# Optimization experiments

Measured on AMD Instinct MI355X. Metric: run time of the kernel, lower is better.

The kernel has to match this reference:

```python
import jax, jax.numpy as jnp
import numpy as np

EPS = 1e-6
LAMBDA_INIT = 0.8

def rmsnorm(x, g):
    return x * jax.lax.rsqrt(jnp.mean(x * x, axis=-1, keepdims=True) + EPS) * g

def diff_attention(q_in, kv_in, Wq, Wk, Wv, Wo, lq1, lk1, lq2, lk2, causal):
    # q_in: [B,T,D], kv_in: [B,S,D]; Wq/Wk: [D, H*2*hs], Wv: [D, H*hs], Wo: [H*hs, D]
    B, T, _ = q_in.shape
    S = kv_in.shape[1]
    H, hs = lq1.shape
    q = (q_in @ Wq).reshape(B, T, H, 2, hs)
    k = (kv_in @ Wk).reshape(B, S, H, 2, hs)
    v = (kv_in @ Wv).reshape(B, S, H, hs)
    q1, q2 = q[..., 0, :], q[..., 1, :]
    k1, k2 = k[..., 0, :], k[..., 1, :]
    scale = 1.0 / np.sqrt(hs).astype(np.float32)
    a1 = jnp.einsum('bthd,bshd->bhts', q1, k1) * scale  # [B,H,T,S]
    a2 = jnp.einsum('bthd,bshd->bhts', q2, k2) * scale
    if causal:
        mask = jnp.tril(jnp.ones((T, S), dtype=bool))
        neg = jnp.asarray(-1e9, a1.dtype)
        a1 = jnp.where(mask, a1, neg)
        a2 = jnp.where(mask, a2, neg)
    s1 = jax.nn.softmax(a1, axis=-1)
    s2 = jax.nn.softmax(a2, axis=-1)
    lam = jnp.exp(jnp.sum(lq1 * lk1, -1)) - jnp.exp(jnp.sum(lq2 * lk2, -1)) + LAMBDA_INIT  # [H]
    attn = s1 - lam[None, :, None, None] * s2
    o = jnp.einsum('bhts,bshd->bthd', attn, v)  # [B,T,H,hs]
    # per-head RMSNorm (no affine) scaled by (1 - lambda_init), per Diff Transformer
    o = o * jax.lax.rsqrt(jnp.mean(o * o, -1, keepdims=True) + EPS) * (1.0 - LAMBDA_INIT)
    return o.reshape(B, T, H * hs) @ Wo

def swiglu(x, W1, W2, W3):
    return (jax.nn.silu(x @ W1) * (x @ W2)) @ W3

def setup_inputs():
    B, T, D, H, hs = 4, 1024, 1024, 16, 64
    Dff = 4 * D
    ks = jax.random.split(jax.random.key(0), 24)
    w = lambda i, shape, s=0.02: (jax.random.normal(ks[i], shape, jnp.float32) * s)
    return {
        'x': jax.random.normal(ks[0], (B, T, D), jnp.float32),
        'encoder_output': jax.random.normal(ks[1], (B, T, D), jnp.float32),
        'Wq_s': w(2, (D, H * 2 * hs)), 'Wk_s': w(3, (D, H * 2 * hs)),
        'Wv_s': w(4, (D, H * hs)), 'Wo_s': w(5, (H * hs, D)),
        'lq1_s': w(6, (H, hs), 0.1), 'lk1_s': w(7, (H, hs), 0.1),
        'lq2_s': w(8, (H, hs), 0.1), 'lk2_s': w(9, (H, hs), 0.1),
        'Wq_c': w(10, (D, H * 2 * hs)), 'Wk_c': w(11, (D, H * 2 * hs)),
        'Wv_c': w(12, (D, H * hs)), 'Wo_c': w(13, (H * hs, D)),
        'lq1_c': w(14, (H, hs), 0.1), 'lk1_c': w(15, (H, hs), 0.1),
        'lq2_c': w(16, (H, hs), 0.1), 'lk2_c': w(17, (H, hs), 0.1),
        'g_rms': jnp.ones((D,), jnp.float32),
        'W1': w(18, (D, Dff)), 'W2': w(19, (D, Dff)), 'W3': w(20, (Dff, D)),
    }

def reference(x, encoder_output, Wq_s, Wk_s, Wv_s, Wo_s, lq1_s, lk1_s, lq2_s, lk2_s,
              Wq_c, Wk_c, Wv_c, Wo_c, lq1_c, lk1_c, lq2_c, lk2_c,
              g_rms, W1, W2, W3):
    # dropout prob 0.0 -> identity (eval/reference mode)
    h = rmsnorm(x, g_rms)
    h = diff_attention(h, h, Wq_s, Wk_s, Wv_s, Wo_s, lq1_s, lk1_s, lq2_s, lk2_s, causal=True) + h
    h = diff_attention(h, encoder_output, Wq_c, Wk_c, Wv_c, Wo_c, lq1_c, lk1_c, lq2_c, lk2_c, causal=False)
    h = h + h  # faithful to source: out = dropout(out) + out after cross-attention
    h = swiglu(rmsnorm(h, g_rms), W1, W2, W3) + h
    return h
```

## Files before the change

### kernel.cpp

```cpp
#include <hip/hip_runtime.h>

typedef __attribute__((ext_vector_type(8))) short s16x8;
typedef __attribute__((ext_vector_type(4))) float f32x4;
typedef unsigned short u16;

__device__ __forceinline__ float bu2f(u16 u) {
    union { unsigned int i; float f; } x; x.i = ((unsigned int)u) << 16; return x.f;
}
__device__ __forceinline__ u16 f2bu(float f) {
    union { float f; unsigned int i; } x; x.f = f;
    unsigned int r = x.i + 0x7fffu + ((x.i >> 16) & 1u);
    return (u16)(r >> 16);
}

__device__ __forceinline__ void gld_lds16(const void* g, void* l) {
    __builtin_amdgcn_global_load_lds(
        (const __attribute__((address_space(1))) unsigned int*)g,
        (__attribute__((address_space(3))) unsigned int*)l, 16, 0, 0);
}
#define WAIT_VM0()   asm volatile("s_waitcnt vmcnt(0)" ::: "memory")
#define WAIT_LGKM0() asm volatile("s_waitcnt lgkmcnt(0)" ::: "memory")
#define MEMBAR()     asm volatile("" ::: "memory")

__global__ __launch_bounds__(256)
void transpose4_k(const float* s0, const float* s1, const float* s2, const float* s3,
                  u16* d0, u16* d1, u16* d2, u16* d3, int R, int C) {
    const float* src = blockIdx.z == 0 ? s0 : blockIdx.z == 1 ? s1 : blockIdx.z == 2 ? s2 : s3;
    u16* dst = blockIdx.z == 0 ? d0 : blockIdx.z == 1 ? d1 : blockIdx.z == 2 ? d2 : d3;
    __shared__ u16 t[32][33];
    int bx = blockIdx.x * 32, by = blockIdx.y * 32;
    int x = bx + threadIdx.x;
#pragma unroll
    for (int k = 0; k < 4; ++k)
        t[threadIdx.y + k * 8][threadIdx.x] = f2bu(src[(size_t)(by + threadIdx.y + k * 8) * C + x]);
    __syncthreads();
    int x2 = by + threadIdx.x;
#pragma unroll
    for (int k = 0; k < 4; ++k)
        dst[(size_t)(bx + threadIdx.y + k * 8) * R + x2] = t[threadIdx.x][threadIdx.y + k * 8];
}

__global__ __launch_bounds__(256)
void convert_k(const float* __restrict__ a, u16* __restrict__ o, int n4) {
    int i = blockIdx.x * 256 + threadIdx.x;
    if (i >= n4) return;
    float4 v = ((const float4*)a)[i];
    ushort4 u;
    u.x = f2bu(v.x); u.y = f2bu(v.y); u.z = f2bu(v.z); u.w = f2bu(v.w);
    ((ushort4*)o)[i] = u;
}

__global__ __launch_bounds__(256)
void rmsnorm_k(const float* __restrict__ x, const float* __restrict__ g, u16* __restrict__ y) {
    const int row = blockIdx.x, tid = threadIdx.x;
    float4 v = ((const float4*)(x + (size_t)row * 1024))[tid];
    float ss = v.x * v.x + v.y * v.y + v.z * v.z + v.w * v.w;
#pragma unroll
    for (int off = 32; off; off >>= 1) ss += __shfl_xor(ss, off, 64);
    __shared__ float red[4];
    if ((tid & 63) == 0) red[tid >> 6] = ss;
    __syncthreads();
    float tot = red[0] + red[1] + red[2] + red[3];
    float sc = rsqrtf(tot * (1.f / 1024.f) + 1e-6f);
    float4 gv = ((const float4*)g)[tid];
    ushort4 o;
    o.x = f2bu(v.x * sc * gv.x);
    o.y = f2bu(v.y * sc * gv.y);
    o.z = f2bu(v.z * sc * gv.z);
    o.w = f2bu(v.w * sc * gv.w);
    ((ushort4*)(y + (size_t)row * 1024))[tid] = o;
}

__global__ __launch_bounds__(256)
void silumul_k(const u16* __restrict__ a, const u16* __restrict__ b, u16* __restrict__ o, int n4) {
    int i = blockIdx.x * 256 + threadIdx.x;
    if (i >= n4) return;
    ushort4 ua = ((const ushort4*)a)[i], ub = ((const ushort4*)b)[i];
    ushort4 uo;
    {
        float v = bu2f(ua.x); uo.x = f2bu(v / (1.f + __expf(-v)) * bu2f(ub.x));
        v = bu2f(ua.y); uo.y = f2bu(v / (1.f + __expf(-v)) * bu2f(ub.y));
        v = bu2f(ua.z); uo.z = f2bu(v / (1.f + __expf(-v)) * bu2f(ub.z));
        v = bu2f(ua.w); uo.w = f2bu(v / (1.f + __expf(-v)) * bu2f(ub.w));
    }
    ((ushort4*)o)[i] = uo;
}

template <int TM>
__global__ __launch_bounds__(256, 2)
void gemm_bt(const u16* __restrict__ A, const u16* __restrict__ Bt, void* __restrict__ C,
             const void* __restrict__ res, int M, int N, int K, int mode) {
    constexpr int MI = TM / 32;
    __shared__ u16 sA[TM * 32];
    __shared__ u16 sB[128 * 32];
    const int tid = threadIdx.x;
    const int w = tid >> 6, lane = tid & 63, q4 = lane >> 4, l16 = lane & 15;
    const int m0 = blockIdx.y * TM, n0 = blockIdx.x * 128;
    const int wm = (w >> 1) * (TM / 2), wn = (w & 1) * 64;

    const f32x4 fzero = {0.f, 0.f, 0.f, 0.f};
    f32x4 acc[MI][4];
#pragma unroll
    for (int i = 0; i < MI; ++i)
#pragma unroll
        for (int j = 0; j < 4; ++j) acc[i][j] = fzero;

    const int r0 = tid >> 2, c0 = (tid & 3) * 8;

    for (int k0 = 0; k0 < K; k0 += 32) {
        gld_lds16(A + (size_t)(m0 + r0) * K + k0 + c0, &sA[tid * 8]);
        if (TM == 128)
            gld_lds16(A + (size_t)(m0 + 64 + r0) * K + k0 + c0, &sA[(256 + tid) * 8]);
        gld_lds16(Bt + (size_t)(n0 + r0) * K + k0 + c0, &sB[tid * 8]);
        gld_lds16(Bt + (size_t)(n0 + 64 + r0) * K + k0 + c0, &sB[(256 + tid) * 8]);
        WAIT_VM0();
        __syncthreads();
        s16x8 af[MI], bfr[4];
#pragma unroll
        for (int i = 0; i < MI; ++i) af[i] = *(const s16x8*)&sA[(wm + i * 16 + l16) * 32 + q4 * 8];
#pragma unroll
        for (int j = 0; j < 4; ++j) bfr[j] = *(const s16x8*)&sB[(wn + j * 16 + l16) * 32 + q4 * 8];
#pragma unroll
        for (int i = 0; i < MI; ++i)
#pragma unroll
            for (int j = 0; j < 4; ++j)
                acc[i][j] = __builtin_amdgcn_mfma_f32_16x16x32_bf16(af[i], bfr[j], acc[i][j], 0, 0, 0);
        __syncthreads();
    }

    const size_t QBSZ = (size_t)4096 * 2048;
    const size_t FSZ  = (size_t)4096 * 4096;
#pragma unroll
    for (int i = 0; i < MI; ++i)
#pragma unroll
        for (int j = 0; j < 4; ++j)
#pragma unroll
            for (int r = 0; r < 4; ++r) {
                int m = m0 + wm + i * 16 + q4 * 4 + r;
                int n = n0 + wn + j * 16 + l16;
                float v = acc[i][j][r];
                if (mode == 0) {
                    ((u16*)C)[(size_t)m * N + n] = f2bu(v);
                } else if (mode == 1) {
                    ((u16*)C)[(size_t)m * N + n] = f2bu(v + bu2f(((const u16*)res)[(size_t)m * N + n]));
                } else if (mode == 2) {
                    ((float*)C)[(size_t)m * N + n] = 2.f * v;
                } else if (mode == 4) {
                    ((float*)C)[(size_t)m * N + n] = v + ((const float*)res)[(size_t)m * N + n];
                } else if (mode == 5) {
                    if (n < 2048) ((u16*)C)[(size_t)m * 2048 + n] = f2bu(v);
                    else if (n < 4096) ((u16*)C)[QBSZ + (size_t)m * 2048 + (n - 2048)] = f2bu(v);
                    else {
                        int nn = n - 4096, hh = nn >> 6, d = nn & 63, b = m >> 10, s = m & 1023;
                        ((u16*)C)[2 * QBSZ + ((size_t)((b * 16 + hh) * 64 + d)) * 1024 + s] = f2bu(v);
                    }
                } else if (mode == 6) {
                    if (n < 2048) ((u16*)C)[(size_t)m * 2048 + n] = f2bu(v);
                    else {
                        int nn = n - 2048, hh = nn >> 6, d = nn & 63, b = m >> 10, s = m & 1023;
                        ((u16*)C)[QBSZ + ((size_t)((b * 16 + hh) * 64 + d)) * 1024 + s] = f2bu(v);
                    }
                } else {
                    if (n < 4096) ((u16*)C)[(size_t)m * 4096 + n] = f2bu(v);
                    else ((u16*)C)[FSZ + (size_t)m * 4096 + (n - 4096)] = f2bu(v);
                }
            }
}

template <bool CAUSAL>
__global__ __launch_bounds__(256, 2)
void diff_flash(const u16* __restrict__ Q, const u16* __restrict__ Kg, const u16* __restrict__ Vt,
                u16* __restrict__ O, const float* __restrict__ lq1, const float* __restrict__ lk1,
                const float* __restrict__ lq2, const float* __restrict__ lk2, int T, int S) {
    __shared__ u16 sK1[2][64 * 64];
    __shared__ u16 sK2[2][64 * 64];
    __shared__ u16 sV[2][64 * 64];
    __shared__ u16 sP[4][16 * 64];

    const int tid = threadIdx.x;
    const int w = tid >> 6, lane = tid & 63, q4 = lane >> 4, l16 = lane & 15;
    const int h = blockIdx.x, b = blockIdx.y;
    const int zt = CAUSAL ? (gridDim.z - 1 - blockIdx.z) : blockIdx.z;
    const int t0 = zt * 64;
    const f32x4 fzero = {0.f, 0.f, 0.f, 0.f};

    float d1 = 0.f, d2 = 0.f;
    for (int d = 0; d < 64; ++d) {
        d1 += lq1[h * 64 + d] * lk1[h * 64 + d];
        d2 += lq2[h * 64 + d] * lk2[h * 64 + d];
    }
    const float lam = __expf(d1) - __expf(d2) + 0.8f;

    s16x8 qf[2][2];
    {
        const size_t qrow = (size_t)(b * T + t0 + w * 16 + l16) * 2048 + h * 128;
#pragma unroll
        for (int c = 0; c < 2; ++c)
#pragma unroll
            for (int kk = 0; kk < 2; ++kk)
                qf[c][kk] = *(const s16x8*)&Q[qrow + c * 64 + kk * 32 + q4 * 8];
    }

    f32x4 o1[4], o2[4];
    float ms1 = -1e30f, ls1 = 0.f, ms2 = -1e30f, ls2 = 0.f;
#pragma unroll
    for (int jn = 0; jn < 4; ++jn) { o1[jn] = fzero; o2[jn] = fzero; }

    const int ntiles = CAUSAL ? (zt + 1) : (S / 64);
    const int rk = tid >> 3;
    const int ckk = (((tid & 7) - rk) & 7) * 8;

    auto stage = [&](int buf, int s0) {
        const size_t kb = (size_t)(b * S + s0 + rk) * 2048 + h * 128;
        gld_lds16(&Kg[kb + ckk], &sK1[buf][tid * 8]);
        gld_lds16(&Kg[kb + (size_t)32 * 2048 + ckk], &sK1[buf][(256 + tid) * 8]);
        gld_lds16(&Kg[kb + 64 + ckk], &sK2[buf][tid * 8]);
        gld_lds16(&Kg[kb + (size_t)32 * 2048 + 64 + ckk], &sK2[buf][(256 + tid) * 8]);
        const size_t vb = (size_t)((b * 16 + h) * 64 + rk) * 1024 + s0;
        gld_lds16(&Vt[vb + ckk], &sV[buf][tid * 8]);
        gld_lds16(&Vt[vb + (size_t)32 * 1024 + ckk], &sV[buf][(256 + tid) * 8]);
    };

    u16* const sPw = sP[w];
    const int slot0 = ((0 * 4 + q4 + l16) & 7) * 8;
    const int slot1 = ((1 * 4 + q4 + l16) & 7) * 8;

    stage(0, 0);
    for (int it = 0; it < ntiles; ++it) {
        WAIT_VM0();
        __syncthreads();
        if (it + 1 < ntiles) stage((it + 1) & 1, (it + 1) * 64);
        const int buf = it & 1, s0 = it * 64;
        const bool diag = CAUSAL && (it == ntiles - 1);

        s16x8 vf[4][2];
#pragma unroll
        for (int jn = 0; jn < 4; ++jn) {
            vf[jn][0] = *(const s16x8*)&sV[buf][(jn * 16 + l16) * 64 + slot0];
            vf[jn][1] = *(const s16x8*)&sV[buf][(jn * 16 + l16) * 64 + slot1];
        }

        auto comp_step = [&](const u16* sK, const s16x8* qkk, float& m, float& l, f32x4* o) {
            f32x4 sc[4];
#pragma unroll
            for (int js = 0; js < 4; ++js) sc[js] = fzero;
#pragma unroll
            for (int js = 0; js < 4; ++js) {
                s16x8 kf0 = *(const s16x8*)&sK[(js * 16 + l16) * 64 + slot0];
                sc[js] = __builtin_amdgcn_mfma_f32_16x16x32_bf16(kf0, qkk[0], sc[js], 0, 0, 0);
                s16x8 kf1 = *(const s16x8*)&sK[(js * 16 + l16) * 64 + slot1];
                sc[js] = __builtin_amdgcn_mfma_f32_16x16x32_bf16(kf1, qkk[1], sc[js], 0, 0, 0);
            }
            float p[4][4];
#pragma unroll
            for (int js = 0; js < 4; ++js)
#pragma unroll
                for (int r = 0; r < 4; ++r) {
                    float v = sc[js][r] * 0.125f;
                    if (diag && (s0 + js * 16 + q4 * 4 + r > t0 + w * 16 + l16)) v = -1e9f;
                    p[js][r] = v;
                }
            float mx = p[0][0];
#pragma unroll
            for (int js = 0; js < 4; ++js)
#pragma unroll
                for (int r = 0; r < 4; ++r) mx = fmaxf(mx, p[js][r]);
            mx = fmaxf(mx, __shfl_xor(mx, 16, 64));
            mx = fmaxf(mx, __shfl_xor(mx, 32, 64));
            float mn = fmaxf(m, mx);
            float alpha = __expf(m - mn);
            m = mn;
            float rs = 0.f;
#pragma unroll
            for (int js = 0; js < 4; ++js)
#pragma unroll
                for (int r = 0; r < 4; ++r) { p[js][r] = __expf(p[js][r] - mn); rs += p[js][r]; }
            rs += __shfl_xor(rs, 16, 64);
            rs += __shfl_xor(rs, 32, 64);
            l = l * alpha + rs;
#pragma unroll
            for (int jn = 0; jn < 4; ++jn) o[jn] *= alpha;
#pragma unroll
            for (int js = 0; js < 4; ++js) {
                ushort4 pk;
                pk.x = f2bu(p[js][0]); pk.y = f2bu(p[js][1]);
                pk.z = f2bu(p[js][2]); pk.w = f2bu(p[js][3]);
                int sl = ((js * 2 + (q4 >> 1) + l16) & 7) * 8 + (q4 & 1) * 4;
                *(ushort4*)&sPw[l16 * 64 + sl] = pk;
            }
            WAIT_LGKM0();
            s16x8 pb0 = *(const s16x8*)&sPw[l16 * 64 + slot0];
            s16x8 pb1 = *(const s16x8*)&sPw[l16 * 64 + slot1];
#pragma unroll
            for (int jn = 0; jn < 4; ++jn) {
                o[jn] = __builtin_amdgcn_mfma_f32_16x16x32_bf16(vf[jn][0], pb0, o[jn], 0, 0, 0);
                o[jn] = __builtin_amdgcn_mfma_f32_16x16x32_bf16(vf[jn][1], pb1, o[jn], 0, 0, 0);
            }
            MEMBAR();
        };
        comp_step(sK1[buf], qf[0], ms1, ls1, o1);
        comp_step(sK2[buf], qf[1], ms2, ls2, o2);
        __syncthreads();
    }

    const float inv1 = 1.f / ls1, inv2 = lam / ls2;
    float val[4][4];
    float ss = 0.f;
#pragma unroll
    for (int jn = 0; jn < 4; ++jn)
#pragma unroll
        for (int r = 0; r < 4; ++r) {
            float v = o1[jn][r] * inv1 - o2[jn][r] * inv2;
            val[jn][r] = v;
            ss += v * v;
        }
    ss += __shfl_xor(ss, 16, 64);
    ss += __shfl_xor(ss, 32, 64);
    const float scl = rsqrtf(ss * (1.f / 64.f) + 1e-6f) * 0.2f;
    const size_t orow = (size_t)(b * T + t0 + w * 16 + l16) * 1024 + h * 64;
#pragma unroll
    for (int jn = 0; jn < 4; ++jn) {
        ushort4 ov;
        ov.x = f2bu(val[jn][0] * scl); ov.y = f2bu(val[jn][1] * scl);
        ov.z = f2bu(val[jn][2] * scl); ov.w = f2bu(val[jn][3] * scl);
        *(ushort4*)&O[orow + jn * 16 + q4 * 4] = ov;
    }
}

extern "C" void kernel_launch(void* const* d_in, const int* in_sizes, int n_in,
                              void* d_out, int out_size, void* d_ws, size_t ws_size,
                              hipStream_t stream) {
    (void)in_sizes; (void)n_in; (void)out_size; (void)ws_size;
    const float* x     = (const float*)d_in[0];
    const float* enc   = (const float*)d_in[1];
    const float* Wq_s  = (const float*)d_in[2];
    const float* Wk_s  = (const float*)d_in[3];
    const float* Wv_s  = (const float*)d_in[4];
    const float* Wo_s  = (const float*)d_in[5];
    const float* lq1_s = (const float*)d_in[6];
    const float* lk1_s = (const float*)d_in[7];
    const float* lq2_s = (const float*)d_in[8];
    const float* lk2_s = (const float*)d_in[9];
    const float* Wq_c  = (const float*)d_in[10];
    const float* Wk_c  = (const float*)d_in[11];
    const float* Wv_c  = (const float*)d_in[12];
    const float* Wo_c  = (const float*)d_in[13];
    const float* lq1_c = (const float*)d_in[14];
    const float* lk1_c = (const float*)d_in[15];
    const float* lq2_c = (const float*)d_in[16];
    const float* lk2_c = (const float*)d_in[17];
    const float* g_rms = (const float*)d_in[18];
    const float* W1    = (const float*)d_in[19];
    const float* W2    = (const float*)d_in[20];
    const float* W3    = (const float*)d_in[21];

    char* ws = (char*)d_ws;
    size_t off = 0;
    auto ab = [&](size_t elems) -> u16* { u16* p = (u16*)(ws + off); off += elems * 2; return p; };
    u16* WqkvTs = ab((size_t)5120 * 1024);
    u16* WoTs   = ab((size_t)1024 * 1024);
    u16* WqTc   = ab((size_t)2048 * 1024);
    u16* WkvTc  = ab((size_t)3072 * 1024);
    u16* WoTc   = ab((size_t)1024 * 1024);
    u16* W12T   = ab((size_t)8192 * 1024);
    u16* W3T    = ab((size_t)1024 * 4096);
    char* pool = ws + off;
    u16* h0   = ab((size_t)4096 * 1024);
    u16* encb = ab((size_t)4096 * 1024);
    u16* Qb   = ab((size_t)4096 * 2048);
    u16* Kb   = ab((size_t)4096 * 2048);
    u16* Vt   = ab((size_t)4096 * 1024);
    u16* Ob   = ab((size_t)4096 * 1024);
    u16* fa   = (u16*)pool;
    u16* fb   = (u16*)(pool + (size_t)4096 * 4096 * 2);
    u16* h1   = ab((size_t)4096 * 1024);
    float* h2 = (float*)(ws + off); off += (size_t)4096 * 1024 * 4;
    u16* rn   = ab((size_t)4096 * 1024);

    dim3 tb(32, 8);
    transpose4_k<<<dim3(64, 32, 4), tb, 0, stream>>>(
        Wq_s, Wk_s, Wq_c, Wk_c,
        WqkvTs, WqkvTs + (size_t)2048 * 1024, WqTc, WkvTc, 1024, 2048);
    transpose4_k<<<dim3(32, 32, 4), tb, 0, stream>>>(
        Wv_s, Wo_s, Wv_c, Wo_c,
        WqkvTs + (size_t)4096 * 1024, WoTs, WkvTc + (size_t)2048 * 1024, WoTc, 1024, 1024);
    transpose4_k<<<dim3(128, 32, 2), tb, 0, stream>>>(
        W1, W2, W1, W2, W12T, W12T + (size_t)4096 * 1024, W12T, W12T, 1024, 4096);
    transpose4_k<<<dim3(32, 128, 1), tb, 0, stream>>>(W3, W3, W3, W3, W3T, W3T, W3T, W3T, 4096, 1024);

    rmsnorm_k<<<4096, 256, 0, stream>>>(x, g_rms, h0);
    convert_k<<<4096, 256, 0, stream>>>(enc, encb, 4096 * 1024 / 4);

    gemm_bt<128><<<dim3(40, 32), 256, 0, stream>>>(h0, WqkvTs, Qb, nullptr, 4096, 5120, 1024, 5);
    diff_flash<true><<<dim3(16, 4, 16), 256, 0, stream>>>(Qb, Kb, Vt, Ob, lq1_s, lk1_s, lq2_s, lk2_s, 1024, 1024);
    gemm_bt<64><<<dim3(8, 64), 256, 0, stream>>>(Ob, WoTs, h1, h0, 4096, 1024, 1024, 1);

    gemm_bt<128><<<dim3(16, 32), 256, 0, stream>>>(h1, WqTc, Qb, nullptr, 4096, 2048, 1024, 0);
    gemm_bt<128><<<dim3(24, 32), 256, 0, stream>>>(encb, WkvTc, Kb, nullptr, 4096, 3072, 1024, 6);
    diff_flash<false><<<dim3(16, 4, 16), 256, 0, stream>>>(Qb, Kb, Vt, Ob, lq1_c, lk1_c, lq2_c, lk2_c, 1024, 1024);
    gemm_bt<64><<<dim3(8, 64), 256, 0, stream>>>(Ob, WoTc, h2, nullptr, 4096, 1024, 1024, 2);

    rmsnorm_k<<<4096, 256, 0, stream>>>(h2, g_rms, rn);
    gemm_bt<128><<<dim3(64, 32), 256, 0, stream>>>(rn, W12T, fa, nullptr, 4096, 8192, 1024, 7);
    silumul_k<<<16384, 256, 0, stream>>>(fa, fb, fa, 4096 * 4096 / 4);
    gemm_bt<64><<<dim3(8, 64), 256, 0, stream>>>(fa, W3T, (float*)d_out, h2, 4096, 1024, 4096, 4);
}
```

Measured before the change: 757.8 us.

## Double-buffer GEMM LDS tiles and drop redundant barriers in GEMM and attention

The GEMM main loop now keeps two LDS buffers for the A and B tiles. It issues the next K-slice's global-to-LDS loads right after the barrier, so they overlap with the current slice's MFMAs. The trailing __syncthreads in both the GEMM and the attention loops is removed and replaced by a single raw s_barrier per iteration, relying on the double buffer for safety. This is meant to hide global load latency and halve barrier count per iteration. The cost is doubled LDS use per GEMM block, which may affect occupancy.

Result: no change. 754.3 us (-0.5%).

```diff
diff --git a/kernel.cpp b/kernel.cpp
--- a/kernel.cpp
+++ b/kernel.cpp
@@ -20,6 +20,7 @@
 }
 #define WAIT_VM0()   asm volatile("s_waitcnt vmcnt(0)" ::: "memory")
 #define WAIT_LGKM0() asm volatile("s_waitcnt lgkmcnt(0)" ::: "memory")
+#define RAW_BARRIER() asm volatile("s_barrier" ::: "memory")
 #define MEMBAR()     asm volatile("" ::: "memory")
 
 __global__ __launch_bounds__(256)
@@ -91,8 +92,8 @@
 void gemm_bt(const u16* __restrict__ A, const u16* __restrict__ Bt, void* __restrict__ C,
              const void* __restrict__ res, int M, int N, int K, int mode) {
     constexpr int MI = TM / 32;
-    __shared__ u16 sA[TM * 32];
-    __shared__ u16 sB[128 * 32];
+    __shared__ u16 sA[2][TM * 32];
+    __shared__ u16 sB[2][128 * 32];
     const int tid = threadIdx.x;
     const int w = tid >> 6, lane = tid & 63, q4 = lane >> 4, l16 = lane & 15;
     const int m0 = blockIdx.y * TM, n0 = blockIdx.x * 128;
@@ -107,25 +108,32 @@
 
     const int r0 = tid >> 2, c0 = (tid & 3) * 8;
 
-    for (int k0 = 0; k0 < K; k0 += 32) {
-        gld_lds16(A + (size_t)(m0 + r0) * K + k0 + c0, &sA[tid * 8]);
+    auto stage = [&](int buf, int k0) {
+        gld_lds16(A + (size_t)(m0 + r0) * K + k0 + c0, &sA[buf][tid * 8]);
         if (TM == 128)
-            gld_lds16(A + (size_t)(m0 + 64 + r0) * K + k0 + c0, &sA[(256 + tid) * 8]);
-        gld_lds16(Bt + (size_t)(n0 + r0) * K + k0 + c0, &sB[tid * 8]);
-        gld_lds16(Bt + (size_t)(n0 + 64 + r0) * K + k0 + c0, &sB[(256 + tid) * 8]);
+            gld_lds16(A + (size_t)(m0 + 64 + r0) * K + k0 + c0, &sA[buf][(256 + tid) * 8]);
+        gld_lds16(Bt + (size_t)(n0 + r0) * K + k0 + c0, &sB[buf][tid * 8]);
+        gld_lds16(Bt + (size_t)(n0 + 64 + r0) * K + k0 + c0, &sB[buf][(256 + tid) * 8]);
+    };
+
+    const int nk = K >> 5;
+    stage(0, 0);
+    for (int it = 0; it < nk; ++it) {
         WAIT_VM0();
-        __syncthreads();
+        RAW_BARRIER();
+        if (it + 1 < nk) stage((it + 1) & 1, (it + 1) * 32);
+        const int buf = it & 1;
         s16x8 af[MI], bfr[4];
 #pragma unroll
-        for (int i = 0; i < MI; ++i) af[i] = *(const s16x8*)&sA[(wm + i * 16 + l16) * 32 + q4 * 8];
-#pragma unroll
-        for (int j = 0; j < 4; ++j) bfr[j] = *(const s16x8*)&sB[(wn + j * 16 + l16) * 32 + q4 * 8];
+        for (int i = 0; i < MI; ++i) af[i] = *(const s16x8*)&sA[buf][(wm + i * 16 + l16) * 32 + q4 * 8];
+#pragma unroll
+        for (int j = 0; j < 4; ++j) bfr[j] = *(const s16x8*)&sB[buf][(wn + j * 16 + l16) * 32 + q4 * 8];
 #pragma unroll
         for (int i = 0; i < MI; ++i)
 #pragma unroll
             for (int j = 0; j < 4; ++j)
                 acc[i][j] = __builtin_amdgcn_mfma_f32_16x16x32_bf16(af[i], bfr[j], acc[i][j], 0, 0, 0);
-        __syncthreads();
+        MEMBAR();
     }
 
     const size_t QBSZ = (size_t)4096 * 2048;
@@ -228,7 +236,7 @@
     stage(0, 0);
     for (int it = 0; it < ntiles; ++it) {
         WAIT_VM0();
-        __syncthreads();
+        RAW_BARRIER();
         if (it + 1 < ntiles) stage((it + 1) & 1, (it + 1) * 64);
         const int buf = it & 1, s0 = it * 64;
         const bool diag = CAUSAL && (it == ntiles - 1);
@@ -300,7 +308,6 @@
         };
         comp_step(sK1[buf], qf[0], ms1, ls1, o1);
         comp_step(sK2[buf], qf[1], ms2, ls2, o2);
-        __syncthreads();
     }
 
     const float inv1 = 1.f / ls1, inv2 = lam / ls2;
```

## Load GEMM fragments directly from global into registers and relax flash barriers

Applied to the files above, without the earlier changes.

The GEMM drops its LDS staging and barriers. Each wave now loads its MFMA fragments straight from global memory into registers, double-buffered over two k-steps, with K fixed at compile time and higher occupancy launch bounds. In the flash attention loop, __syncthreads becomes a raw s_barrier and the end-of-iteration barrier is removed. This cuts LDS traffic and synchronisation, but loses cross-wave data sharing through LDS (more redundant global/L2 reads), and may create a race on the double-buffered K/V tiles.

Measured after the change: 1.200 ms. 58.4% more time.

```diff
diff --git a/kernel.cpp b/kernel.cpp
--- a/kernel.cpp
+++ b/kernel.cpp
@@ -18,8 +18,12 @@
         (const __attribute__((address_space(1))) unsigned int*)g,
         (__attribute__((address_space(3))) unsigned int*)l, 16, 0, 0);
 }
+__device__ __forceinline__ s16x8 ld16g(const u16* p) {
+    return *(const s16x8*)__builtin_assume_aligned(p, 16);
+}
 #define WAIT_VM0()   asm volatile("s_waitcnt vmcnt(0)" ::: "memory")
 #define WAIT_LGKM0() asm volatile("s_waitcnt lgkmcnt(0)" ::: "memory")
+#define RAW_BARRIER() asm volatile("s_barrier" ::: "memory")
 #define MEMBAR()     asm volatile("" ::: "memory")
 
 __global__ __launch_bounds__(256)
@@ -86,13 +90,12 @@
     ((ushort4*)o)[i] = uo;
 }
 
-template <int TM>
-__global__ __launch_bounds__(256, 2)
+template <int TM, int KK>
+__global__ __launch_bounds__(256, (TM == 128 ? 3 : 4))
 void gemm_bt(const u16* __restrict__ A, const u16* __restrict__ Bt, void* __restrict__ C,
-             const void* __restrict__ res, int M, int N, int K, int mode) {
+             const void* __restrict__ res, int M, int N, int mode) {
     constexpr int MI = TM / 32;
-    __shared__ u16 sA[TM * 32];
-    __shared__ u16 sB[128 * 32];
+    constexpr int nk = KK >> 5;
     const int tid = threadIdx.x;
     const int w = tid >> 6, lane = tid & 63, q4 = lane >> 4, l16 = lane & 15;
     const int m0 = blockIdx.y * TM, n0 = blockIdx.x * 128;
@@ -105,28 +108,50 @@
 #pragma unroll
         for (int j = 0; j < 4; ++j) acc[i][j] = fzero;
 
-    const int r0 = tid >> 2, c0 = (tid & 3) * 8;
-
-    for (int k0 = 0; k0 < K; k0 += 32) {
-        gld_lds16(A + (size_t)(m0 + r0) * K + k0 + c0, &sA[tid * 8]);
-        if (TM == 128)
-            gld_lds16(A + (size_t)(m0 + 64 + r0) * K + k0 + c0, &sA[(256 + tid) * 8]);
-        gld_lds16(Bt + (size_t)(n0 + r0) * K + k0 + c0, &sB[tid * 8]);
-        gld_lds16(Bt + (size_t)(n0 + 64 + r0) * K + k0 + c0, &sB[(256 + tid) * 8]);
-        WAIT_VM0();
-        __syncthreads();
-        s16x8 af[MI], bfr[4];
-#pragma unroll
-        for (int i = 0; i < MI; ++i) af[i] = *(const s16x8*)&sA[(wm + i * 16 + l16) * 32 + q4 * 8];
-#pragma unroll
-        for (int j = 0; j < 4; ++j) bfr[j] = *(const s16x8*)&sB[(wn + j * 16 + l16) * 32 + q4 * 8];
+    const u16* ap = A + (size_t)(m0 + wm + l16) * KK + q4 * 8;
+    const u16* bp = Bt + (size_t)(n0 + wn + l16) * KK + q4 * 8;
+
+    s16x8 a0[MI], b0[4], a1[MI], b1[4];
+#pragma unroll
+    for (int i = 0; i < MI; ++i) a0[i] = ld16g(ap + (size_t)i * 16 * KK);
+#pragma unroll
+    for (int j = 0; j < 4; ++j) b0[j] = ld16g(bp + (size_t)j * 16 * KK);
+#pragma unroll
+    for (int i = 0; i < MI; ++i) a1[i] = ld16g(ap + 32 + (size_t)i * 16 * KK);
+#pragma unroll
+    for (int j = 0; j < 4; ++j) b1[j] = ld16g(bp + 32 + (size_t)j * 16 * KK);
+
+    for (int it = 0; it < nk - 2; it += 2) {
 #pragma unroll
         for (int i = 0; i < MI; ++i)
 #pragma unroll
             for (int j = 0; j < 4; ++j)
-                acc[i][j] = __builtin_amdgcn_mfma_f32_16x16x32_bf16(af[i], bfr[j], acc[i][j], 0, 0, 0);
-        __syncthreads();
-    }
+                acc[i][j] = __builtin_amdgcn_mfma_f32_16x16x32_bf16(a0[i], b0[j], acc[i][j], 0, 0, 0);
+        ap += 64; bp += 64;
+#pragma unroll
+        for (int i = 0; i < MI; ++i) a0[i] = ld16g(ap + (size_t)i * 16 * KK);
+#pragma unroll
+        for (int j = 0; j < 4; ++j) b0[j] = ld16g(bp + (size_t)j * 16 * KK);
+#pragma unroll
+        for (int i = 0; i < MI; ++i)
+#pragma unroll
+            for (int j = 0; j < 4; ++j)
+                acc[i][j] = __builtin_amdgcn_mfma_f32_16x16x32_bf16(a1[i], b1[j], acc[i][j], 0, 0, 0);
+#pragma unroll
+        for (int i = 0; i < MI; ++i) a1[i] = ld16g(ap + 32 + (size_t)i * 16 * KK);
+#pragma unroll
+        for (int j = 0; j < 4; ++j) b1[j] = ld16g(bp + 32 + (size_t)j * 16 * KK);
+    }
+#pragma unroll
+    for (int i = 0; i < MI; ++i)
+#pragma unroll
+        for (int j = 0; j < 4; ++j)
+            acc[i][j] = __builtin_amdgcn_mfma_f32_16x16x32_bf16(a0[i], b0[j], acc[i][j], 0, 0, 0);
+#pragma unroll
+    for (int i = 0; i < MI; ++i)
+#pragma unroll
+        for (int j = 0; j < 4; ++j)
+            acc[i][j] = __builtin_amdgcn_mfma_f32_16x16x32_bf16(a1[i], b1[j], acc[i][j], 0, 0, 0);
 
     const size_t QBSZ = (size_t)4096 * 2048;
     const size_t FSZ  = (size_t)4096 * 4096;
@@ -228,7 +253,7 @@
     stage(0, 0);
     for (int it = 0; it < ntiles; ++it) {
         WAIT_VM0();
-        __syncthreads();
+        RAW_BARRIER();
         if (it + 1 < ntiles) stage((it + 1) & 1, (it + 1) * 64);
         const int buf = it & 1, s0 = it * 64;
         const bool diag = CAUSAL && (it == ntiles - 1);
@@ -300,7 +325,6 @@
         };
         comp_step(sK1[buf], qf[0], ms1, ls1, o1);
         comp_step(sK2[buf], qf[1], ms2, ls2, o2);
-        __syncthreads();
     }
 
     const float inv1 = 1.f / ls1, inv2 = lam / ls2;
@@ -391,17 +415,17 @@
     rmsnorm_k<<<4096, 256, 0, stream>>>(x, g_rms, h0);
     convert_k<<<4096, 256, 0, stream>>>(enc, encb, 4096 * 1024 / 4);
 
-    gemm_bt<128><<<dim3(40, 32), 256, 0, stream>>>(h0, WqkvTs, Qb, nullptr, 4096, 5120, 1024, 5);
+    gemm_bt<128, 1024><<<dim3(40, 32), 256, 0, stream>>>(h0, WqkvTs, Qb, nullptr, 4096, 5120, 5);
     diff_flash<true><<<dim3(16, 4, 16), 256, 0, stream>>>(Qb, Kb, Vt, Ob, lq1_s, lk1_s, lq2_s, lk2_s, 1024, 1024);
-    gemm_bt<64><<<dim3(8, 64), 256, 0, stream>>>(Ob, WoTs, h1, h0, 4096, 1024, 1024, 1);
-
-    gemm_bt<128><<<dim3(16, 32), 256, 0, stream>>>(h1, WqTc, Qb, nullptr, 4096, 2048, 1024, 0);
-    gemm_bt<128><<<dim3(24, 32), 256, 0, stream>>>(encb, WkvTc, Kb, nullptr, 4096, 3072, 1024, 6);
+    gemm_bt<64, 1024><<<dim3(8, 64), 256, 0, stream>>>(Ob, WoTs, h1, h0, 4096, 1024, 1);
+
+    gemm_bt<128, 1024><<<dim3(16, 32), 256, 0, stream>>>(h1, WqTc, Qb, nullptr, 4096, 2048, 0);
+    gemm_bt<128, 1024><<<dim3(24, 32), 256, 0, stream>>>(encb, WkvTc, Kb, nullptr, 4096, 3072, 6);
     diff_flash<false><<<dim3(16, 4, 16), 256, 0, stream>>>(Qb, Kb, Vt, Ob, lq1_c, lk1_c, lq2_c, lk2_c, 1024, 1024);
-    gemm_bt<64><<<dim3(8, 64), 256, 0, stream>>>(Ob, WoTc, h2, nullptr, 4096, 1024, 1024, 2);
+    gemm_bt<64, 1024><<<dim3(8, 64), 256, 0, stream>>>(Ob, WoTc, h2, nullptr, 4096, 1024, 2);
 
     rmsnorm_k<<<4096, 256, 0, stream>>>(h2, g_rms, rn);
-    gemm_bt<128><<<dim3(64, 32), 256, 0, stream>>>(rn, W12T, fa, nullptr, 4096, 8192, 1024, 7);
+    gemm_bt<128, 1024><<<dim3(64, 32), 256, 0, stream>>>(rn, W12T, fa, nullptr, 4096, 8192, 7);
     silumul_k<<<16384, 256, 0, stream>>>(fa, fb, fa, 4096 * 4096 / 4);
-    gemm_bt<64><<<dim3(8, 64), 256, 0, stream>>>(fa, W3T, (float*)d_out, h2, 4096, 1024, 4096, 4);
-}
+    gemm_bt<64, 4096><<<dim3(8, 64), 256, 0, stream>>>(fa, W3T, (float*)d_out, h2, 4096, 1024, 4);
+}
```
